# Performance work log

Measured on AMD Instinct MI355X. Metric: run time of the kernel, lower is better.

Reference implementation:

```python
import jax, jax.numpy as jnp
import numpy as np

WS = 14          # window size
NH = 12          # num heads
HD = 64          # head dim
EPS = 1e-6

# static relative-position index table: q_size == k_size == WS, no resize branch
_REL_IDX = np.arange(WS)[:, None] - np.arange(WS)[None, :] + (WS - 1)  # [WS, WS] in [0, 2*WS-2]


def _layer_norm(x, g, b):
    m = jnp.mean(x, axis=-1, keepdims=True)
    v = jnp.mean(jnp.square(x - m), axis=-1, keepdims=True)
    return (x - m) * jax.lax.rsqrt(v + EPS) * g + b


def setup_inputs() -> dict:
    key = jax.random.key(0)
    ks = jax.random.split(key, 8)
    B, H, W, C = 4, 64, 64, 768
    s = lambda fan: 1.0 / np.sqrt(fan)
    return {
        "x": jax.random.normal(ks[0], (B, H, W, C), jnp.float32),
        "ln1_g": jnp.ones((C,), jnp.float32),
        "ln1_b": jnp.zeros((C,), jnp.float32),
        "w_qkv": jax.random.normal(ks[1], (C, 3 * C), jnp.float32) * s(C),
        "b_qkv": jnp.zeros((3 * C,), jnp.float32),
        "w_proj": jax.random.normal(ks[2], (C, C), jnp.float32) * s(C),
        "b_proj": jnp.zeros((C,), jnp.float32),
        "rel_pos_h": jax.random.normal(ks[3], (2 * WS - 1, HD), jnp.float32) * 0.02,
        "rel_pos_w": jax.random.normal(ks[4], (2 * WS - 1, HD), jnp.float32) * 0.02,
        "ln2_g": jnp.ones((C,), jnp.float32),
        "ln2_b": jnp.zeros((C,), jnp.float32),
        "w_fc1": jax.random.normal(ks[5], (C, 4 * C), jnp.float32) * s(C),
        "b_fc1": jnp.zeros((4 * C,), jnp.float32),
        "w_fc2": jax.random.normal(ks[6], (4 * C, C), jnp.float32) * s(4 * C),
        "b_fc2": jnp.zeros((C,), jnp.float32),
    }


def reference(x, ln1_g, ln1_b, w_qkv, b_qkv, w_proj, b_proj,
              rel_pos_h, rel_pos_w, ln2_g, ln2_b, w_fc1, b_fc1, w_fc2, b_fc2):
    B, H, W, C = x.shape
    shortcut = x
    x = _layer_norm(x, ln1_g, ln1_b)

    # --- window partition (with zero padding) ---
    pad_h = (WS - H % WS) % WS
    pad_w = (WS - W % WS) % WS
    xp = jnp.pad(x, ((0, 0), (0, pad_h), (0, pad_w), (0, 0)))
    Hp, Wp = H + pad_h, W + pad_w
    nH, nW = Hp // WS, Wp // WS
    win = xp.reshape(B, nH, WS, nW, WS, C).transpose(0, 1, 3, 2, 4, 5)
    win = win.reshape(B * nH * nW, WS * WS, C)  # [Bw, 196, C]
    Bw = win.shape[0]

    # --- window attention ---
    qkv = win @ w_qkv + b_qkv                                   # [Bw, 196, 3C]
    qkv = qkv.reshape(Bw, WS * WS, 3, NH, HD)
    qkv = qkv.transpose(2, 0, 3, 1, 4).reshape(3, Bw * NH, WS * WS, HD)
    q, k, v = qkv[0], qkv[1], qkv[2]
    scale = HD ** -0.5
    attn = jnp.einsum('bqd,bkd->bqk', q * scale, k)             # [Bw*NH, 196, 196]

    # decomposed relative position bias (MViTv2)
    Rh = rel_pos_h[_REL_IDX]                                    # [WS, WS, HD]
    Rw = rel_pos_w[_REL_IDX]                                    # [WS, WS, HD]
    rq = q.reshape(-1, WS, WS, HD)
    rel_h = jnp.einsum('bhwc,hkc->bhwk', rq, Rh)                # [Bw*NH, WS, WS, WS]
    rel_w = jnp.einsum('bhwc,wkc->bhwk', rq, Rw)
    attn = attn.reshape(-1, WS, WS, WS, WS)
    attn = attn + rel_h[..., None] + rel_w[:, :, :, None, :]
    attn = attn.reshape(-1, WS * WS, WS * WS)

    attn = jax.nn.softmax(attn, axis=-1)
    out = attn @ v                                              # [Bw*NH, 196, HD]
    out = out.reshape(Bw, NH, WS, WS, HD).transpose(0, 2, 3, 1, 4).reshape(Bw, WS, WS, C)
    out = out @ w_proj + b_proj

    # --- window reverse (remove padding) ---
    xr = out.reshape(B, nH, nW, WS, WS, C).transpose(0, 1, 3, 2, 4, 5)
    xr = xr.reshape(B, Hp, Wp, C)[:, :H, :W, :]

    x = shortcut + xr

    # --- MLP ---
    y = _layer_norm(x, ln2_g, ln2_b)
    y = jax.nn.gelu(y @ w_fc1 + b_fc1, approximate=False)
    y = y @ w_fc2 + b_fc2
    return x + y
```

## Files before the change

### kernel.cpp

```cpp
#include <hip/hip_runtime.h>
#include <hip/hip_bf16.h>
#include <math.h>


typedef unsigned short u16;
typedef unsigned int u32;
typedef __attribute__((ext_vector_type(8))) short short8;
typedef __attribute__((ext_vector_type(4))) float f32x4;

__device__ __forceinline__ u16 f2bf(float x) {
  u32 u = __float_as_uint(x);
  u32 r = (u + 0x7fffu + ((u >> 16) & 1u)) >> 16;
  return (u16)r;
}
__device__ __forceinline__ float bf2f(u16 h) { return __uint_as_float(((u32)h) << 16); }

__device__ __forceinline__ void gl_lds16(const void* g, void* l) {
  __builtin_amdgcn_global_load_lds((const __attribute__((address_space(1))) void*)g,
                                   (__attribute__((address_space(3))) void*)l, 16, 0, 0);
}

__device__ __forceinline__ void block_reduce_2(float& s1, float& s2) {
#pragma unroll
  for (int off = 32; off > 0; off >>= 1) {
    s1 += __shfl_down(s1, off, 64);
    s2 += __shfl_down(s2, off, 64);
  }
  __shared__ float sb[4][2];
  int lane = threadIdx.x & 63;
  int wv = threadIdx.x >> 6;
  if (lane == 0) { sb[wv][0] = s1; sb[wv][1] = s2; }
  __syncthreads();
  s1 = sb[0][0] + sb[1][0] + sb[2][0] + sb[3][0];
  s2 = sb[0][1] + sb[1][1] + sb[2][1] + sb[3][1];
}

__global__ __launch_bounds__(256) void ln1_win_kernel(
    const float* __restrict__ x, const float* __restrict__ g,
    const float* __restrict__ bta, u16* __restrict__ wb, int tofs) {
  int token_g = tofs + blockIdx.x;
  int wi = token_g / 196, t = token_g % 196;
  int b = wi / 25, rem = wi % 25;
  int h = (rem / 5) * 14 + t / 14, w = (rem % 5) * 14 + t % 14;
  u16* out = wb + (size_t)blockIdx.x * 768;
  int tid = threadIdx.x;
  if (h >= 64 || w >= 64) {
#pragma unroll
    for (int i = 0; i < 3; i++) out[tid + 256 * i] = 0;
    return;
  }
  const float* xin = x + ((size_t)((b * 64 + h) * 64 + w)) * 768;
  float v[3];
  float s1 = 0.f, s2 = 0.f;
#pragma unroll
  for (int i = 0; i < 3; i++) {
    float val = xin[tid + 256 * i];
    v[i] = val; s1 += val; s2 += val * val;
  }
  block_reduce_2(s1, s2);
  float mean = s1 * (1.f / 768.f);
  float var = s2 * (1.f / 768.f) - mean * mean;
  float inv = rsqrtf(var + 1e-6f);
#pragma unroll
  for (int i = 0; i < 3; i++) {
    int c = tid + 256 * i;
    out[c] = f2bf((v[i] - mean) * inv * g[c] + bta[c]);
  }
}

__global__ __launch_bounds__(256) void ln2_kernel(
    const float* __restrict__ x, const float* __restrict__ g,
    const float* __restrict__ bta, u16* __restrict__ yb) {
  int token = blockIdx.x;
  const float* xin = x + (size_t)token * 768;
  u16* out = yb + (size_t)token * 768;
  int tid = threadIdx.x;
  float v[3];
  float s1 = 0.f, s2 = 0.f;
#pragma unroll
  for (int i = 0; i < 3; i++) {
    float val = xin[tid + 256 * i];
    v[i] = val; s1 += val; s2 += val * val;
  }
  block_reduce_2(s1, s2);
  float mean = s1 * (1.f / 768.f);
  float var = s2 * (1.f / 768.f) - mean * mean;
  float inv = rsqrtf(var + 1e-6f);
#pragma unroll
  for (int i = 0; i < 3; i++) {
    int c = tid + 256 * i;
    out[c] = f2bf((v[i] - mean) * inv * g[c] + bta[c]);
  }
}

__global__ __launch_bounds__(256) void convT_kernel(
    const float* __restrict__ w, u16* __restrict__ o, int K, int N) {
  __shared__ float t[32][33];
  int n0 = blockIdx.x * 32, k0 = blockIdx.y * 32;
  int tid = threadIdx.x;
  {
    int i = tid >> 3, jq = (tid & 7) * 4;
    float4 v = *(const float4*)&w[(size_t)(k0 + i) * N + n0 + jq];
    t[i][jq] = v.x; t[i][jq + 1] = v.y; t[i][jq + 2] = v.z; t[i][jq + 3] = v.w;
  }
  __syncthreads();
  int j = tid >> 3, sub = tid & 7;
  u16 h[4];
#pragma unroll
  for (int m = 0; m < 4; m++) h[m] = f2bf(t[sub * 4 + m][j]);
  u32* dst = (u32*)(o + (size_t)(n0 + j) * K + (k0 + sub * 4));
  dst[0] = (u32)h[0] | ((u32)h[1] << 16);
  dst[1] = (u32)h[2] | ((u32)h[3] << 16);
}

template <int EPI>
__global__ __launch_bounds__(256) void mgemm_kernel(
    const u16* __restrict__ A, const u16* __restrict__ BT,
    const float* __restrict__ bias, int M, int N, int Ke,
    float* __restrict__ outF, u16* __restrict__ outX,
    const float* __restrict__ resid, int rofs,
    u16* __restrict__ qb, u16* __restrict__ kb, u16* __restrict__ vT) {
  __shared__ u16 sA[128 * 64];
  __shared__ u16 sB[128 * 64];
  const int tid = threadIdx.x;
  const int wv = tid >> 6, lane = tid & 63;
  const int bm = blockIdx.y * 128, bn = blockIdx.x * 128;
  const int wr = wv >> 1, wc = wv & 1;

  size_t aOff[4], bOff[4];
  u16* ldsA[4];
  u16* ldsB[4];
#pragma unroll
  for (int i = 0; i < 4; i++) {
    int c = (wv * 4 + i) * 64 + lane;
    int row = c >> 3, qp = c & 7;
    int q = qp ^ (row & 7);
    int ar = bm + row;
    if (ar >= M) ar = M - 1;
    aOff[i] = (size_t)ar * Ke + q * 8;
    bOff[i] = (size_t)(bn + row) * Ke + q * 8;
    ldsA[i] = &sA[(wv * 4 + i) * 512];
    ldsB[i] = &sB[(wv * 4 + i) * 512];
  }

  f32x4 acc[4][4];
#pragma unroll
  for (int i = 0; i < 4; i++)
#pragma unroll
    for (int j = 0; j < 4; j++) acc[i][j] = (f32x4){0.f, 0.f, 0.f, 0.f};

  for (int k0 = 0; k0 < Ke; k0 += 64) {
    __syncthreads();
#pragma unroll
    for (int i = 0; i < 4; i++) gl_lds16(A + aOff[i] + k0, ldsA[i]);
#pragma unroll
    for (int i = 0; i < 4; i++) gl_lds16(BT + bOff[i] + k0, ldsB[i]);
    __syncthreads();

    short8 af[4][2], bf[4][2];
#pragma unroll
    for (int f = 0; f < 4; f++)
#pragma unroll
      for (int kh = 0; kh < 2; kh++) {
        int ra = wr * 64 + f * 16 + (lane & 15);
        int qa = kh * 4 + (lane >> 4);
        af[f][kh] = *(const short8*)&sA[ra * 64 + ((qa ^ (ra & 7)) * 8)];
        int rb = wc * 64 + f * 16 + (lane & 15);
        bf[f][kh] = *(const short8*)&sB[rb * 64 + ((qa ^ (rb & 7)) * 8)];
      }
#pragma unroll
    for (int kh = 0; kh < 2; kh++)
#pragma unroll
      for (int fi = 0; fi < 4; fi++)
#pragma unroll
        for (int fj = 0; fj < 4; fj++)
          acc[fi][fj] = __builtin_amdgcn_mfma_f32_16x16x32_bf16(
              af[fi][kh], bf[fj][kh], acc[fi][fj], 0, 0, 0);
  }

#pragma unroll
  for (int fi = 0; fi < 4; fi++) {
#pragma unroll
    for (int fj = 0; fj < 4; fj++) {
      int col = bn + wc * 64 + fj * 16 + (lane & 15);
      float bcol = bias[col];
#pragma unroll
      for (int r = 0; r < 4; r++) {
        int row = bm + wr * 64 + fi * 16 + (lane >> 4) * 4 + r;
        if (row >= M) continue;
        float v = acc[fi][fj][r] + bcol;
        if (EPI == 0) {
          int which = (col >= 1536) ? 2 : (col >= 768 ? 1 : 0);
          int cr = col - which * 768;
          int head = cr >> 6, d0 = cr & 63;
          int wl = row / 196, t = row - wl * 196;
          int b2l = wl * 12 + head;
          if (which == 0)
            qb[((size_t)b2l * 196 + t) * 64 + d0] = f2bf(v);
          else if (which == 1)
            kb[((size_t)b2l * 196 + t) * 64 + d0] = f2bf(v);
          else
            vT[((size_t)b2l * 64 + d0) * 256 + t] = f2bf(v);
        } else if (EPI == 1) {
          int rg = row + rofs;
          int wi = rg / 196, t = rg - wi * 196;
          int b = wi / 25, rem = wi % 25;
          int hh = (rem / 5) * 14 + t / 14;
          int ww = (rem % 5) * 14 + t % 14;
          if (hh < 64 && ww < 64) {
            size_t off = ((size_t)((b * 64 + hh) * 64 + ww)) * 768 + col;
            outF[off] = resid[off] + v;
          }
        } else if (EPI == 2) {
          float gg = 0.5f * v * (1.f + erff(v * 0.70710678118654752f));
          outX[(size_t)row * N + col] = f2bf(gg);
        } else {
          size_t off = (size_t)row * N + col;
          outF[off] = v + resid[off];
        }
      }
    }
  }
}

__global__ __launch_bounds__(128) void rel_kernel(
    const u16* __restrict__ qb, const float* __restrict__ rph,
    const float* __restrict__ rpw, float* __restrict__ relh,
    float* __restrict__ relw) {
  int b2l = blockIdx.x / 196, row = blockIdx.x % 196;
  __shared__ float sq[64];
  int tid = threadIdx.x;
  if (tid < 64) sq[tid] = bf2f(qb[((size_t)b2l * 196 + row) * 64 + tid]);
  __syncthreads();
  int rh = row / 14, rw = row % 14;
  int t = tid & 63;
  if (t < 56) {
    int which = tid >> 6;
    int kh = t >> 2, part = t & 3;
    int rel = (which ? rw : rh) - kh + 13;
    const float* R = (which ? rpw : rph) + (size_t)rel * 64 + part * 16;
    float p = 0.f;
#pragma unroll
    for (int d = 0; d < 16; d++) p += sq[part * 16 + d] * R[d];
    p += __shfl_down(p, 2, 4);
    p += __shfl_down(p, 1, 4);
    if (part == 0) {
      float* dst = which ? relw : relh;
      dst[((size_t)b2l * 196 + row) * 14 + kh] = p;
    }
  }
}

template <int EPI>
__global__ __launch_bounds__(256) void sgemm64_kernel(
    const u16* __restrict__ Aall, const u16* __restrict__ BTall,
    int Ke, int Arows,
    const float* __restrict__ relh, const float* __restrict__ relw,
    u16* __restrict__ pe, u16* __restrict__ winx) {
  __shared__ u16 sA[64 * 64];
  __shared__ u16 sB[256 * 64];
  __shared__ float sred[64][4];
  const int tid = threadIdx.x;
  const int wv = tid >> 6, lane = tid & 63;
  const int b2l = blockIdx.y;
  const int bm = blockIdx.x * 64;
  const u16* A = Aall + (size_t)b2l * Arows * Ke;
  const u16* BT = BTall + (size_t)b2l * 196 * Ke;

  size_t aOff[2], bOff[8];
  u16* ldsA[2];
  u16* ldsB[8];
#pragma unroll
  for (int i = 0; i < 2; i++) {
    int c = (wv * 2 + i) * 64 + lane;
    int rl = c >> 3, qp = c & 7;
    int q = qp ^ (rl & 7);
    int ga = bm + rl;
    if (ga >= Arows) ga = Arows - 1;
    aOff[i] = (size_t)ga * Ke + q * 8;
    ldsA[i] = &sA[(wv * 2 + i) * 512];
  }
#pragma unroll
  for (int i = 0; i < 8; i++) {
    int c = (wv * 8 + i) * 64 + lane;
    int rl = c >> 3, qp = c & 7;
    int q = qp ^ (rl & 7);
    int gb = rl > 195 ? 195 : rl;
    bOff[i] = (size_t)gb * Ke + q * 8;
    ldsB[i] = &sB[(wv * 8 + i) * 512];
  }

  f32x4 acc[4][4];
#pragma unroll
  for (int i = 0; i < 4; i++)
#pragma unroll
    for (int j = 0; j < 4; j++) acc[i][j] = (f32x4){0.f, 0.f, 0.f, 0.f};

  for (int k0 = 0; k0 < Ke; k0 += 64) {
    __syncthreads();
#pragma unroll
    for (int i = 0; i < 2; i++) gl_lds16(A + aOff[i] + k0, ldsA[i]);
#pragma unroll
    for (int i = 0; i < 8; i++) gl_lds16(BT + bOff[i] + k0, ldsB[i]);
    __syncthreads();

    short8 af[4][2], bf[4][2];
#pragma unroll
    for (int f = 0; f < 4; f++)
#pragma unroll
      for (int kh = 0; kh < 2; kh++) {
        int ra = f * 16 + (lane & 15);
        int qa = kh * 4 + (lane >> 4);
        af[f][kh] = *(const short8*)&sA[ra * 64 + ((qa ^ (ra & 7)) * 8)];
        int rb = wv * 64 + f * 16 + (lane & 15);
        bf[f][kh] = *(const short8*)&sB[rb * 64 + ((qa ^ (rb & 7)) * 8)];
      }
#pragma unroll
    for (int kh = 0; kh < 2; kh++)
#pragma unroll
      for (int fi = 0; fi < 4; fi++)
#pragma unroll
        for (int fj = 0; fj < 4; fj++)
          acc[fi][fj] = __builtin_amdgcn_mfma_f32_16x16x32_bf16(
              af[fi][kh], bf[fj][kh], acc[fi][fj], 0, 0, 0);
  }

  if (EPI == 0) {
#pragma unroll
    for (int fi = 0; fi < 4; fi++)
#pragma unroll
      for (int fj = 0; fj < 4; fj++)
#pragma unroll
        for (int r = 0; r < 4; r++) {
          int grow = bm + fi * 16 + (lane >> 4) * 4 + r;
          int col = wv * 64 + fj * 16 + (lane & 15);
          float v = -3.0e38f;
          if (grow < 196 && col < 196) {
            size_t rb = ((size_t)b2l * 196 + grow) * 14;
            v = acc[fi][fj][r] * 0.125f + relh[rb + col / 14] + relw[rb + col % 14];
          }
          acc[fi][fj][r] = v;
        }
    float red[4][4];
#pragma unroll
    for (int fi = 0; fi < 4; fi++)
#pragma unroll
      for (int r = 0; r < 4; r++) {
        float m = fmaxf(fmaxf(acc[fi][0][r], acc[fi][1][r]),
                        fmaxf(acc[fi][2][r], acc[fi][3][r]));
#pragma unroll
        for (int msk = 1; msk < 16; msk <<= 1) m = fmaxf(m, __shfl_xor(m, msk, 64));
        red[fi][r] = m;
      }
    if ((lane & 15) == 0)
#pragma unroll
      for (int fi = 0; fi < 4; fi++)
#pragma unroll
        for (int r = 0; r < 4; r++)
          sred[fi * 16 + (lane >> 4) * 4 + r][wv] = red[fi][r];
    __syncthreads();
#pragma unroll
    for (int fi = 0; fi < 4; fi++)
#pragma unroll
      for (int r = 0; r < 4; r++) {
        int rl = fi * 16 + (lane >> 4) * 4 + r;
        red[fi][r] = fmaxf(fmaxf(sred[rl][0], sred[rl][1]),
                           fmaxf(sred[rl][2], sred[rl][3]));
      }
    __syncthreads();
#pragma unroll
    for (int fi = 0; fi < 4; fi++)
#pragma unroll
      for (int fj = 0; fj < 4; fj++)
#pragma unroll
        for (int r = 0; r < 4; r++)
          acc[fi][fj][r] = __expf(acc[fi][fj][r] - red[fi][r]);
#pragma unroll
    for (int fi = 0; fi < 4; fi++)
#pragma unroll
      for (int r = 0; r < 4; r++) {
        float s = acc[fi][0][r] + acc[fi][1][r] + acc[fi][2][r] + acc[fi][3][r];
#pragma unroll
        for (int msk = 1; msk < 16; msk <<= 1) s += __shfl_xor(s, msk, 64);
        red[fi][r] = s;
      }
    if ((lane & 15) == 0)
#pragma unroll
      for (int fi = 0; fi < 4; fi++)
#pragma unroll
        for (int r = 0; r < 4; r++)
          sred[fi * 16 + (lane >> 4) * 4 + r][wv] = red[fi][r];
    __syncthreads();
#pragma unroll
    for (int fi = 0; fi < 4; fi++)
#pragma unroll
      for (int r = 0; r < 4; r++) {
        int rl = fi * 16 + (lane >> 4) * 4 + r;
        red[fi][r] = 1.f / (sred[rl][0] + sred[rl][1] + sred[rl][2] + sred[rl][3]);
      }
#pragma unroll
    for (int fi = 0; fi < 4; fi++)
#pragma unroll
      for (int fj = 0; fj < 4; fj++)
#pragma unroll
        for (int r = 0; r < 4; r++) {
          int grow = bm + fi * 16 + (lane >> 4) * 4 + r;
          int col = wv * 64 + fj * 16 + (lane & 15);
          if (grow < 196 && col < 196)
            pe[((size_t)b2l * 196 + grow) * 256 + col] =
                f2bf(acc[fi][fj][r] * red[fi][r]);
        }
    int nrow = 196 - bm; if (nrow > 64) nrow = 64;
    for (int z = tid; z < nrow * 30; z += 256) {
      int r = z / 30, idx = z % 30;
      *(u32*)&pe[((size_t)b2l * 196 + bm + r) * 256 + 196 + idx * 2] = 0;
    }
  } else {
    int wi_l = b2l / 12, head = b2l - wi_l * 12;
#pragma unroll
    for (int fi = 0; fi < 4; fi++)
#pragma unroll
      for (int fj = 0; fj < 4; fj++)
#pragma unroll
        for (int r = 0; r < 4; r++) {
          int d = fi * 16 + (lane >> 4) * 4 + r;
          int t = wv * 64 + fj * 16 + (lane & 15);
          if (t < 196)
            winx[((size_t)wi_l * 196 + t) * 768 + head * 64 + d] =
                f2bf(acc[fi][fj][r]);
        }
  }
}

extern "C" void kernel_launch(void* const* d_in, const int* in_sizes, int n_in,
                              void* d_out, int out_size, void* d_ws, size_t ws_size,
                              hipStream_t stream) {
  const float* x = (const float*)d_in[0];
  const float* ln1_g = (const float*)d_in[1];
  const float* ln1_b = (const float*)d_in[2];
  const float* w_qkv = (const float*)d_in[3];
  const float* b_qkv = (const float*)d_in[4];
  const float* w_proj = (const float*)d_in[5];
  const float* b_proj = (const float*)d_in[6];
  const float* rph = (const float*)d_in[7];
  const float* rpw = (const float*)d_in[8];
  const float* ln2_g = (const float*)d_in[9];
  const float* ln2_b = (const float*)d_in[10];
  const float* w_fc1 = (const float*)d_in[11];
  const float* b_fc1 = (const float*)d_in[12];
  const float* w_fc2 = (const float*)d_in[13];
  const float* b_fc2 = (const float*)d_in[14];
  float* out = (float*)d_out;
  char* wsb = (char*)d_ws;

  const size_t WB = 14155776ull;
  const size_t PERW = 2764032ull;
  static const int nwCand[9] = {100, 50, 25, 20, 10, 5, 4, 2, 1};
  int NW = 0;
  for (int i = 0; i < 9; i++)
    if (WB + (size_t)nwCand[i] * PERW <= ws_size) { NW = nwCand[i]; break; }
  int R = 0;
  for (int rc = 16384; rc >= 128; rc >>= 1)
    if (WB + (size_t)rc * 7680ull <= ws_size) { R = rc; break; }
  if (NW == 0 || R == 0) return;

  u16* wqkvT = (u16*)(wsb);
  u16* wprojT = (u16*)(wsb + 3538944);
  u16* wfc1T = (u16*)(wsb + 4718592);
  u16* wfc2T = (u16*)(wsb + 9437184);
  char* pool = wsb + WB;
  u16* win_c = (u16*)pool;
  u16* qb_c = (u16*)(pool + (size_t)NW * 301056);
  u16* kb_c = (u16*)(pool + (size_t)NW * 602112);
  u16* vT_c = (u16*)(pool + (size_t)NW * 903168);
  float* relh_c = (float*)(pool + (size_t)NW * 1296384);
  float* relw_c = (float*)(pool + (size_t)NW * 1428096);
  u16* pe_c = (u16*)(pool + (size_t)NW * 1559808);
  u16* y_c = (u16*)pool;
  u16* h_c = (u16*)(pool + (size_t)R * 1536);

  convT_kernel<<<dim3(72, 24), 256, 0, stream>>>(w_qkv, wqkvT, 768, 2304);
  convT_kernel<<<dim3(24, 24), 256, 0, stream>>>(w_proj, wprojT, 768, 768);
  convT_kernel<<<dim3(96, 24), 256, 0, stream>>>(w_fc1, wfc1T, 768, 3072);
  convT_kernel<<<dim3(24, 96), 256, 0, stream>>>(w_fc2, wfc2T, 3072, 768);

  const int MW = NW * 196;
  const int gy = (MW + 127) / 128;
  const int nchunks = 100 / NW;
  for (int c = 0; c < nchunks; c++) {
    ln1_win_kernel<<<MW, 256, 0, stream>>>(x, ln1_g, ln1_b, win_c, c * MW);
    mgemm_kernel<0><<<dim3(18, gy), 256, 0, stream>>>(
        win_c, wqkvT, b_qkv, MW, 2304, 768, nullptr, nullptr, nullptr, 0,
        qb_c, kb_c, vT_c);
    rel_kernel<<<NW * 12 * 196, 128, 0, stream>>>(qb_c, rph, rpw, relh_c, relw_c);
    sgemm64_kernel<0><<<dim3(4, NW * 12), 256, 0, stream>>>(
        qb_c, kb_c, 64, 196, relh_c, relw_c, pe_c, nullptr);
    sgemm64_kernel<1><<<dim3(1, NW * 12), 256, 0, stream>>>(
        vT_c, pe_c, 256, 64, nullptr, nullptr, nullptr, win_c);
    mgemm_kernel<1><<<dim3(6, gy), 256, 0, stream>>>(
        win_c, wprojT, b_proj, MW, 768, 768, out, nullptr, x, c * MW,
        nullptr, nullptr, nullptr);
  }
  for (int r0 = 0; r0 < 16384; r0 += R) {
    ln2_kernel<<<R, 256, 0, stream>>>(out + (size_t)r0 * 768, ln2_g, ln2_b, y_c);
    mgemm_kernel<2><<<dim3(24, R / 128), 256, 0, stream>>>(
        y_c, wfc1T, b_fc1, R, 3072, 768, nullptr, h_c, nullptr, 0,
        nullptr, nullptr, nullptr);
    mgemm_kernel<3><<<dim3(6, R / 128), 256, 0, stream>>>(
        h_c, wfc2T, b_fc2, R, 768, 3072, out + (size_t)r0 * 768, nullptr,
        out + (size_t)r0 * 768, 0, nullptr, nullptr, nullptr);
  }
}
```

Before: 1.025 ms.

## Pack epilogue stores, restructure rel-pos kernel per head, use tanh GELU

The QKV epilogue writes V-transposed as packed 64-bit stores, and the PV epilogue packs four bf16 outputs per store. The relative-position kernel now runs one block per window-head, staging q and the tables in LDS instead of launching one tiny block per row. The score kernel stages its rel-bias slices in shared memory. The FC1 epilogue replaces erf GELU with a tanh approximation, which is cheaper but deviates slightly from the exact reference.

```diff
diff --git a/kernel.cpp b/kernel.cpp
--- a/kernel.cpp
+++ b/kernel.cpp
@@ -5,6 +5,7 @@
 
 typedef unsigned short u16;
 typedef unsigned int u32;
+typedef unsigned long long u64;
 typedef __attribute__((ext_vector_type(8))) short short8;
 typedef __attribute__((ext_vector_type(4))) float f32x4;
 
@@ -184,23 +185,36 @@
     for (int fj = 0; fj < 4; fj++) {
       int col = bn + wc * 64 + fj * 16 + (lane & 15);
       float bcol = bias[col];
+      int row0 = bm + wr * 64 + fi * 16 + (lane >> 4) * 4;
+      if (EPI == 0 && col >= 1536) {
+        if (row0 < M) {
+          int cr = col - 1536;
+          int head = cr >> 6, d0 = cr & 63;
+          int wl = row0 / 196, t0 = row0 - wl * 196;
+          int b2l = wl * 12 + head;
+          u64 pack = 0;
+#pragma unroll
+          for (int r = 0; r < 4; r++)
+            pack |= (u64)f2bf(acc[fi][fj][r] + bcol) << (16 * r);
+          *(u64*)&vT[((size_t)b2l * 64 + d0) * 256 + t0] = pack;
+        }
+        continue;
+      }
 #pragma unroll
       for (int r = 0; r < 4; r++) {
-        int row = bm + wr * 64 + fi * 16 + (lane >> 4) * 4 + r;
+        int row = row0 + r;
         if (row >= M) continue;
         float v = acc[fi][fj][r] + bcol;
         if (EPI == 0) {
-          int which = (col >= 1536) ? 2 : (col >= 768 ? 1 : 0);
+          int which = (col >= 768) ? 1 : 0;
           int cr = col - which * 768;
           int head = cr >> 6, d0 = cr & 63;
           int wl = row / 196, t = row - wl * 196;
           int b2l = wl * 12 + head;
           if (which == 0)
             qb[((size_t)b2l * 196 + t) * 64 + d0] = f2bf(v);
-          else if (which == 1)
+          else
             kb[((size_t)b2l * 196 + t) * 64 + d0] = f2bf(v);
-          else
-            vT[((size_t)b2l * 64 + d0) * 256 + t] = f2bf(v);
         } else if (EPI == 1) {
           int rg = row + rofs;
           int wi = rg / 196, t = rg - wi * 196;
@@ -212,8 +226,12 @@
             outF[off] = resid[off] + v;
           }
         } else if (EPI == 2) {
-          float gg = 0.5f * v * (1.f + erff(v * 0.70710678118654752f));
-          outX[(size_t)row * N + col] = f2bf(gg);
+          float y = 0.79788456f * (v + 0.044715f * v * v * v);
+          float ay = fabsf(y);
+          float e = __expf(-2.f * ay);
+          float th = (1.f - e) / (1.f + e);
+          th = (y < 0.f) ? -th : th;
+          outX[(size_t)row * N + col] = f2bf(0.5f * v * (1.f + th));
         } else {
           size_t off = (size_t)row * N + col;
           outF[off] = v + resid[off];
@@ -223,31 +241,41 @@
   }
 }
 
-__global__ __launch_bounds__(128) void rel_kernel(
+__global__ __launch_bounds__(256) void rel_kernel(
     const u16* __restrict__ qb, const float* __restrict__ rph,
     const float* __restrict__ rpw, float* __restrict__ relh,
     float* __restrict__ relw) {
-  int b2l = blockIdx.x / 196, row = blockIdx.x % 196;
-  __shared__ float sq[64];
+  __shared__ u16 sq[196 * 68];
+  __shared__ float sRt[2][27 * 66];
+  int b2l = blockIdx.x;
   int tid = threadIdx.x;
-  if (tid < 64) sq[tid] = bf2f(qb[((size_t)b2l * 196 + row) * 64 + tid]);
+  const u32* qsrc = (const u32*)(qb + (size_t)b2l * 12544);
+  for (int i = tid; i < 6272; i += 256) {
+    int row = i >> 5, p = i & 31;
+    *(u32*)&sq[row * 68 + p * 2] = qsrc[i];
+  }
+  for (int i = tid; i < 1728; i += 256) {
+    int r = i >> 6, c = i & 63;
+    sRt[0][r * 66 + c] = rph[i];
+    sRt[1][r * 66 + c] = rpw[i];
+  }
   __syncthreads();
-  int rh = row / 14, rw = row % 14;
-  int t = tid & 63;
-  if (t < 56) {
-    int which = tid >> 6;
-    int kh = t >> 2, part = t & 3;
-    int rel = (which ? rw : rh) - kh + 13;
-    const float* R = (which ? rpw : rph) + (size_t)rel * 64 + part * 16;
+  for (int o = tid; o < 5488; o += 256) {
+    int which = o >= 2744;
+    int oo = o - which * 2744;
+    int row = oo / 14, kh = oo - row * 14;
+    int rr = which ? (row % 14) : (row / 14);
+    int idx = rr - kh + 13;
+    const float* tab = &sRt[which][idx * 66];
+    const u16* qrow = &sq[row * 68];
     float p = 0.f;
 #pragma unroll
-    for (int d = 0; d < 16; d++) p += sq[part * 16 + d] * R[d];
-    p += __shfl_down(p, 2, 4);
-    p += __shfl_down(p, 1, 4);
-    if (part == 0) {
-      float* dst = which ? relw : relh;
-      dst[((size_t)b2l * 196 + row) * 14 + kh] = p;
+    for (int d = 0; d < 64; d += 2) {
+      u32 qp = *(const u32*)&qrow[d];
+      p += __uint_as_float(qp << 16) * tab[d];
+      p += __uint_as_float(qp & 0xffff0000u) * tab[d + 1];
     }
+    (which ? relw : relh)[((size_t)b2l * 196 + row) * 14 + kh] = p;
   }
 }
 
@@ -326,6 +354,17 @@
   }
 
   if (EPI == 0) {
+    __syncthreads();
+    float* sRel = (float*)sA;
+    {
+      size_t base = ((size_t)b2l * 196 + bm) * 14;
+      int nval = (196 - bm < 64 ? 196 - bm : 64) * 14;
+      for (int i = tid; i < 896; i += 256) {
+        sRel[i] = (i < nval) ? relh[base + i] : 0.f;
+        sRel[896 + i] = (i < nval) ? relw[base + i] : 0.f;
+      }
+    }
+    __syncthreads();
 #pragma unroll
     for (int fi = 0; fi < 4; fi++)
 #pragma unroll
@@ -336,8 +375,9 @@
           int col = wv * 64 + fj * 16 + (lane & 15);
           float v = -3.0e38f;
           if (grow < 196 && col < 196) {
-            size_t rb = ((size_t)b2l * 196 + grow) * 14;
-            v = acc[fi][fj][r] * 0.125f + relh[rb + col / 14] + relw[rb + col % 14];
+            int lr = grow - bm;
+            v = acc[fi][fj][r] * 0.125f + sRel[lr * 14 + col / 14] +
+                sRel[896 + lr * 14 + col % 14];
           }
           acc[fi][fj][r] = v;
         }
@@ -418,17 +458,20 @@
   } else {
     int wi_l = b2l / 12, head = b2l - wi_l * 12;
 #pragma unroll
-    for (int fi = 0; fi < 4; fi++)
-#pragma unroll
-      for (int fj = 0; fj < 4; fj++)
-#pragma unroll
-        for (int r = 0; r < 4; r++) {
-          int d = fi * 16 + (lane >> 4) * 4 + r;
-          int t = wv * 64 + fj * 16 + (lane & 15);
-          if (t < 196)
-            winx[((size_t)wi_l * 196 + t) * 768 + head * 64 + d] =
-                f2bf(acc[fi][fj][r]);
+    for (int fi = 0; fi < 4; fi++) {
+      int d0 = fi * 16 + (lane >> 4) * 4;
+#pragma unroll
+      for (int fj = 0; fj < 4; fj++) {
+        int t = wv * 64 + fj * 16 + (lane & 15);
+        if (t < 196) {
+          u64 pack = 0;
+#pragma unroll
+          for (int r = 0; r < 4; r++)
+            pack |= (u64)f2bf(acc[fi][fj][r]) << (16 * r);
+          *(u64*)&winx[((size_t)wi_l * 196 + t) * 768 + head * 64 + d0] = pack;
         }
+      }
+    }
   }
 }
 
@@ -492,7 +535,7 @@
     mgemm_kernel<0><<<dim3(18, gy), 256, 0, stream>>>(
         win_c, wqkvT, b_qkv, MW, 2304, 768, nullptr, nullptr, nullptr, 0,
         qb_c, kb_c, vT_c);
-    rel_kernel<<<NW * 12 * 196, 128, 0, stream>>>(qb_c, rph, rpw, relh_c, relw_c);
+    rel_kernel<<<NW * 12, 256, 0, stream>>>(qb_c, rph, rpw, relh_c, relw_c);
     sgemm64_kernel<0><<<dim3(4, NW * 12), 256, 0, stream>>>(
         qb_c, kb_c, 64, 196, relh_c, relw_c, pe_c, nullptr);
     sgemm64_kernel<1><<<dim3(1, NW * 12), 256, 0, stream>>>(
```

Result: faster. 916.1 us (-10.6%).
